# Optimization experiments

Hardware: AMD Instinct MI355X
Metric: run time of the kernel (lower is better)

## Reference

```python
import jax, jax.numpy as jnp
import numpy as np

N_NODES = 100000
N_EDGES = 1600000
D_IN = 128
D_OUT = 128


def setup_inputs() -> dict:
    key = jax.random.key(0)
    k1, k2, k3, k4 = jax.random.split(key, 4)
    x = jax.random.normal(k1, (N_NODES, D_IN), dtype=jnp.float32)
    # Xavier-uniform-like init for weight (exact distribution irrelevant for correctness baseline)
    weight = jax.random.normal(k2, (D_IN, D_OUT), dtype=jnp.float32) * (1.0 / np.sqrt(D_IN))
    bias = jnp.zeros((D_OUT,), dtype=jnp.float32)
    edge_index = jax.random.randint(k3, (2, N_EDGES), 0, N_NODES, dtype=jnp.int64 if jax.config.read('jax_enable_x64') else jnp.int32)
    edge_weight = jax.random.uniform(k4, (N_EDGES,), dtype=jnp.float32)
    return {"x": x, "weight": weight, "bias": bias,
            "edge_index": edge_index, "edge_weight": edge_weight}


def reference(x, weight, bias, edge_index, edge_weight):
    # support = X @ W   -- dense projection [N, D_out]
    support = x @ weight
    # output = A @ support -- SpMM via gather + weighted segment-sum
    src = edge_index[1]  # column index of adj (neighbor being aggregated)
    dst = edge_index[0]  # row index of adj (node receiving the message)
    messages = support[src] * edge_weight[:, None]          # [E, D_out]
    out = jax.ops.segment_sum(messages, dst, num_segments=N_NODES)  # [N, D_out]
    return out + bias
```

## Files before the change

kernel.cpp:

```cpp
#include <hip/hip_runtime.h>
#include <hip/hip_bf16.h>

#define N_NODES 100000
#define N_EDGES 1600000
#define D 128

#define NBUK 1024
#define BSH 7
#define CAP 2560
#define CAP_H 1344
#define NAGG2 (((N_NODES + 127) >> BSH) * 2)
#define NSCAT 512
#define PA_EPB 3125
#define SRC_MASK 0x01FFFFFF

typedef __attribute__((ext_vector_type(8))) short bf16x8;
typedef __attribute__((ext_vector_type(4))) float f32x4;

static __device__ __forceinline__ short f2bf(float f) {
    unsigned u = __builtin_bit_cast(unsigned, f);
    u += 0x7FFFu + ((u >> 16) & 1u);
    return (short)(u >> 16);
}
static __device__ __forceinline__ float bf2f(unsigned short h) {
    unsigned u = ((unsigned)h) << 16;
    return __builtin_bit_cast(float, u);
}

__global__ void wt_kernel(const float* __restrict__ w, short* __restrict__ wt,
                          int* __restrict__ gcur) {
    const int i = blockIdx.x * blockDim.x + threadIdx.x;
    if (i < D * D) {
        const int k = i / D, c = i % D;
        wt[c * D + k] = f2bf(w[i]);
    }
    if (i < NBUK) gcur[i] = 0;
}

__global__ __launch_bounds__(256) void gemm_mfma_kernel(
    const float* __restrict__ x, const short* __restrict__ wt,
    short* __restrict__ sup) {
    const int wid = blockIdx.x * 4 + (threadIdx.x >> 6);
    if (wid >= N_NODES / 16) return;
    const int l = threadIdx.x & 63;
    const int r = l & 15, g = l >> 4;
    const size_t row0 = (size_t)wid * 16;

    bf16x8 a[4];
    const float* xp = x + (row0 + r) * D + g * 8;
#pragma unroll
    for (int ks = 0; ks < 4; ++ks) {
        const float4 f0 = *reinterpret_cast<const float4*>(xp + ks * 32);
        const float4 f1 = *reinterpret_cast<const float4*>(xp + ks * 32 + 4);
        bf16x8 t;
        t[0] = f2bf(f0.x); t[1] = f2bf(f0.y); t[2] = f2bf(f0.z); t[3] = f2bf(f0.w);
        t[4] = f2bf(f1.x); t[5] = f2bf(f1.y); t[6] = f2bf(f1.z); t[7] = f2bf(f1.w);
        a[ks] = t;
    }

#pragma unroll
    for (int nt = 0; nt < 8; ++nt) {
        f32x4 acc = {0.f, 0.f, 0.f, 0.f};
        const short* wp = wt + (size_t)(nt * 16 + r) * D + g * 8;
#pragma unroll
        for (int ks = 0; ks < 4; ++ks) {
            const bf16x8 b = *reinterpret_cast<const bf16x8*>(wp + ks * 32);
            acc = __builtin_amdgcn_mfma_f32_16x16x32_bf16(a[ks], b, acc, 0, 0, 0);
        }
        short* sp = sup + (row0 + g * 4) * D + nt * 16 + r;
#pragma unroll
        for (int q = 0; q < 4; ++q) sp[q * D] = f2bf(acc[q]);
    }
}

__global__ __launch_bounds__(1024) void bukscatter_kernel(
    const int* __restrict__ dst, const int* __restrict__ src,
    const float* __restrict__ ew, int* __restrict__ gcur,
    int2* __restrict__ inter_sw) {
    __shared__ int h[NBUK];
    const int t = threadIdx.x;
    if (t < NBUK) h[t] = 0;
    __syncthreads();
    const int beg = blockIdx.x * PA_EPB;
    const int end = min(beg + PA_EPB, N_EDGES);
    for (int i = beg + t; i < end; i += 1024)
        atomicAdd(&h[dst[i] >> BSH], 1);
    __syncthreads();
    if (t < NBUK) {
        const int c = h[t];
        h[t] = c ? (t * CAP + atomicAdd(&gcur[t], c)) : 0;
    }
    __syncthreads();
    for (int i = beg + t; i < end; i += 1024) {
        const int d = dst[i];
        const int pos = atomicAdd(&h[d >> BSH], 1);
        inter_sw[pos] = make_int2(src[i] | ((d & 127) << 25),
                                  __float_as_int(ew[i]));
    }
}

__global__ __launch_bounds__(512) void sortagg_kernel(
    const int* __restrict__ gcur, const int2* __restrict__ inter_sw,
    const short* __restrict__ sup, const float* __restrict__ bias,
    float* __restrict__ out) {
    __shared__ int2 eb[CAP_H];
    __shared__ int st[64];
    __shared__ int cur[64];
    const int b = blockIdx.x, t = threadIdx.x;
    const int cb = b >> 1, hf = b & 1;
    const int cnt = gcur[cb];
    const int2* in = inter_sw + (size_t)cb * CAP;

    if (t < 64) st[t] = 0;
    __syncthreads();

    int2 e0, e1, e2, e3, e4;
    bool k0 = false, k1 = false, k2 = false, k3 = false, k4 = false;
    const int i0 = t, i1 = t + 512, i2 = t + 1024, i3 = t + 1536, i4 = t + 2048;
    if (i0 < cnt) { e0 = in[i0]; const int d7 = (unsigned)e0.x >> 25; if ((d7 >> 6) == hf) { k0 = true; atomicAdd(&st[d7 & 63], 1); } }
    if (i1 < cnt) { e1 = in[i1]; const int d7 = (unsigned)e1.x >> 25; if ((d7 >> 6) == hf) { k1 = true; atomicAdd(&st[d7 & 63], 1); } }
    if (i2 < cnt) { e2 = in[i2]; const int d7 = (unsigned)e2.x >> 25; if ((d7 >> 6) == hf) { k2 = true; atomicAdd(&st[d7 & 63], 1); } }
    if (i3 < cnt) { e3 = in[i3]; const int d7 = (unsigned)e3.x >> 25; if ((d7 >> 6) == hf) { k3 = true; atomicAdd(&st[d7 & 63], 1); } }
    if (i4 < cnt) { e4 = in[i4]; const int d7 = (unsigned)e4.x >> 25; if ((d7 >> 6) == hf) { k4 = true; atomicAdd(&st[d7 & 63], 1); } }
    __syncthreads();

    if (t < 64) {
        const int hv = st[t];
        int s = hv;
#pragma unroll
        for (int o = 1; o < 64; o <<= 1) {
            const int v = __shfl_up(s, o);
            if (t >= o) s += v;
        }
        st[t] = s - hv;
        cur[t] = s - hv;
    }
    __syncthreads();

    if (k0) eb[atomicAdd(&cur[((unsigned)e0.x >> 25) & 63], 1)] = make_int2(e0.x & SRC_MASK, e0.y);
    if (k1) eb[atomicAdd(&cur[((unsigned)e1.x >> 25) & 63], 1)] = make_int2(e1.x & SRC_MASK, e1.y);
    if (k2) eb[atomicAdd(&cur[((unsigned)e2.x >> 25) & 63], 1)] = make_int2(e2.x & SRC_MASK, e2.y);
    if (k3) eb[atomicAdd(&cur[((unsigned)e3.x >> 25) & 63], 1)] = make_int2(e3.x & SRC_MASK, e3.y);
    if (k4) eb[atomicAdd(&cur[((unsigned)e4.x >> 25) & 63], 1)] = make_int2(e4.x & SRC_MASK, e4.y);
    __syncthreads();

    const int wv = t >> 6, lane = t & 63;
    const int g = lane >> 4;
    const int fl = lane & 15;
    const int node0 = (cb << BSH) + (hf << 6);

    const float4 b0 = *reinterpret_cast<const float4*>(&bias[fl * 8]);
    const float4 b1 = *reinterpret_cast<const float4*>(&bias[fl * 8 + 4]);

    for (int k = 0; k < 8; ++k) {
        const int nl = wv * 8 + k;
        const int node = node0 + nl;
        if (node >= N_NODES) break;
        const int beg = st[nl], end = cur[nl];

        float acc[8] = {0, 0, 0, 0, 0, 0, 0, 0};
        for (int i = beg + g; i < end; i += 4) {
            const int2 sw = eb[i];
            const float w = __int_as_float(sw.y);
            const bf16x8 v = *reinterpret_cast<const bf16x8*>(
                &sup[(size_t)sw.x * D + fl * 8]);
#pragma unroll
            for (int q = 0; q < 8; ++q)
                acc[q] = fmaf(w, bf2f((unsigned short)v[q]), acc[q]);
        }
#pragma unroll
        for (int q = 0; q < 8; ++q) {
            acc[q] += __shfl_xor(acc[q], 16);
            acc[q] += __shfl_xor(acc[q], 32);
        }
        if (g == 0) {
            float* o = &out[(size_t)node * D + fl * 8];
            reinterpret_cast<float4*>(o)[0] =
                make_float4(acc[0] + b0.x, acc[1] + b0.y, acc[2] + b0.z, acc[3] + b0.w);
            reinterpret_cast<float4*>(o)[1] =
                make_float4(acc[4] + b1.x, acc[5] + b1.y, acc[6] + b1.z, acc[7] + b1.w);
        }
    }
}

extern "C" void kernel_launch(void* const* d_in, const int* in_sizes, int n_in,
                              void* d_out, int out_size, void* d_ws, size_t ws_size,
                              hipStream_t stream) {
    const float* x      = (const float*)d_in[0];
    const float* weight = (const float*)d_in[1];
    const float* bias   = (const float*)d_in[2];
    const int*   eidx   = (const int*)d_in[3];
    const float* ew     = (const float*)d_in[4];
    float* out = (float*)d_out;

    const int* dst_idx = eidx;
    const int* src_idx = eidx + N_EDGES;

    char* p = (char*)d_ws;
    short* sup       = (short*)p;  p += (size_t)N_NODES * D * 2;
    short* wt        = (short*)p;  p += (size_t)D * D * 2;
    int*   gcur      = (int*)p;    p += NBUK * 4;
    int2*  inter_sw  = (int2*)p;   p += (size_t)NBUK * CAP * 8;

    wt_kernel<<<(D * D + 255) / 256, 256, 0, stream>>>(weight, wt, gcur);

    gemm_mfma_kernel<<<(N_NODES / 16 + 3) / 4, 256, 0, stream>>>(x, wt, sup);

    bukscatter_kernel<<<NSCAT, 1024, 0, stream>>>(dst_idx, src_idx, ew, gcur,
                                                  inter_sw);

    sortagg_kernel<<<NAGG2, 512, 0, stream>>>(gcur, inter_sw, sup, bias, out);
}
```

Baseline: 134.2 us.

## Quantize projected features to int8 with per-row scales folded into edge weights

Adds a pass that quantizes the bf16 support matrix to int8 with a per-row absmax scale. The per-row scale is multiplied into each edge weight during bucket scatter, so the gather in aggregation reads 8 bytes per lane instead of 16. The aim is to halve gather traffic in the memory-bound SpMM. The cost is an extra kernel and a random scale lookup per edge in the scatter. The workspace is reorganized so inter_sw aliases the bf16 buffer, and the scatter block count is halved. Int8 quantization also loosens accuracy further than bf16.

```diff
diff --git a/kernel.cpp b/kernel.cpp
--- a/kernel.cpp
+++ b/kernel.cpp
@@ -10,8 +10,8 @@
 #define CAP 2560
 #define CAP_H 1344
 #define NAGG2 (((N_NODES + 127) >> BSH) * 2)
-#define NSCAT 512
-#define PA_EPB 3125
+#define NSCAT 256
+#define PA_EPB 6250
 #define SRC_MASK 0x01FFFFFF
 
 typedef __attribute__((ext_vector_type(8))) short bf16x8;
@@ -39,7 +39,7 @@
 
 __global__ __launch_bounds__(256) void gemm_mfma_kernel(
     const float* __restrict__ x, const short* __restrict__ wt,
-    short* __restrict__ sup) {
+    short* __restrict__ sup16) {
     const int wid = blockIdx.x * 4 + (threadIdx.x >> 6);
     if (wid >= N_NODES / 16) return;
     const int l = threadIdx.x & 63;
@@ -67,16 +67,40 @@
             const bf16x8 b = *reinterpret_cast<const bf16x8*>(wp + ks * 32);
             acc = __builtin_amdgcn_mfma_f32_16x16x32_bf16(a[ks], b, acc, 0, 0, 0);
         }
-        short* sp = sup + (row0 + g * 4) * D + nt * 16 + r;
+        short* sp = sup16 + (row0 + g * 4) * D + nt * 16 + r;
 #pragma unroll
         for (int q = 0; q < 4; ++q) sp[q * D] = f2bf(acc[q]);
     }
+}
+
+__global__ __launch_bounds__(256) void quant_kernel(
+    const short* __restrict__ sup16, signed char* __restrict__ sup8,
+    float* __restrict__ scales) {
+    const int row = blockIdx.x * 4 + (threadIdx.x >> 6);
+    if (row >= N_NODES) return;
+    const int lane = threadIdx.x & 63;
+
+    const unsigned v = *reinterpret_cast<const unsigned*>(
+        &sup16[(size_t)row * D + lane * 2]);
+    const float a = bf2f((unsigned short)(v & 0xFFFFu));
+    const float b = bf2f((unsigned short)(v >> 16));
+    float m = fmaxf(fabsf(a), fabsf(b));
+#pragma unroll
+    for (int o = 1; o < 64; o <<= 1) m = fmaxf(m, __shfl_xor(m, o));
+
+    const float inv = (m > 0.f) ? 127.f / m : 0.f;
+    const int qa = __float2int_rn(a * inv);
+    const int qb = __float2int_rn(b * inv);
+    const unsigned short packed =
+        (unsigned short)((qa & 0xFF) | ((qb & 0xFF) << 8));
+    *reinterpret_cast<unsigned short*>(&sup8[(size_t)row * D + lane * 2]) = packed;
+    if (lane == 0) scales[row] = m * (1.f / 127.f);
 }
 
 __global__ __launch_bounds__(1024) void bukscatter_kernel(
     const int* __restrict__ dst, const int* __restrict__ src,
-    const float* __restrict__ ew, int* __restrict__ gcur,
-    int2* __restrict__ inter_sw) {
+    const float* __restrict__ ew, const float* __restrict__ scales,
+    int* __restrict__ gcur, int2* __restrict__ inter_sw) {
     __shared__ int h[NBUK];
     const int t = threadIdx.x;
     if (t < NBUK) h[t] = 0;
@@ -93,15 +117,16 @@
     __syncthreads();
     for (int i = beg + t; i < end; i += 1024) {
         const int d = dst[i];
+        const int s = src[i];
         const int pos = atomicAdd(&h[d >> BSH], 1);
-        inter_sw[pos] = make_int2(src[i] | ((d & 127) << 25),
-                                  __float_as_int(ew[i]));
+        inter_sw[pos] = make_int2(s | ((d & 127) << 25),
+                                  __float_as_int(ew[i] * scales[s]));
     }
 }
 
 __global__ __launch_bounds__(512) void sortagg_kernel(
     const int* __restrict__ gcur, const int2* __restrict__ inter_sw,
-    const short* __restrict__ sup, const float* __restrict__ bias,
+    const signed char* __restrict__ sup8, const float* __restrict__ bias,
     float* __restrict__ out) {
     __shared__ int2 eb[CAP_H];
     __shared__ int st[64];
@@ -162,11 +187,12 @@
         for (int i = beg + g; i < end; i += 4) {
             const int2 sw = eb[i];
             const float w = __int_as_float(sw.y);
-            const bf16x8 v = *reinterpret_cast<const bf16x8*>(
-                &sup[(size_t)sw.x * D + fl * 8]);
+            const unsigned long long v =
+                *reinterpret_cast<const unsigned long long*>(
+                    &sup8[(size_t)sw.x * D + fl * 8]);
 #pragma unroll
             for (int q = 0; q < 8; ++q)
-                acc[q] = fmaf(w, bf2f((unsigned short)v[q]), acc[q]);
+                acc[q] = fmaf(w, (float)((signed char)(v >> (8 * q))), acc[q]);
         }
 #pragma unroll
         for (int q = 0; q < 8; ++q) {
@@ -197,17 +223,22 @@
     const int* src_idx = eidx + N_EDGES;
 
     char* p = (char*)d_ws;
-    short* sup       = (short*)p;  p += (size_t)N_NODES * D * 2;
+    short* sup16     = (short*)p;
+    int2*  inter_sw  = (int2*)p;
+    p += (size_t)N_NODES * D * 2;
+    signed char* sup8 = (signed char*)p; p += (size_t)N_NODES * D;
+    float* scales    = (float*)p;  p += (size_t)N_NODES * 4;
     short* wt        = (short*)p;  p += (size_t)D * D * 2;
     int*   gcur      = (int*)p;    p += NBUK * 4;
-    int2*  inter_sw  = (int2*)p;   p += (size_t)NBUK * CAP * 8;
 
     wt_kernel<<<(D * D + 255) / 256, 256, 0, stream>>>(weight, wt, gcur);
 
-    gemm_mfma_kernel<<<(N_NODES / 16 + 3) / 4, 256, 0, stream>>>(x, wt, sup);
-
-    bukscatter_kernel<<<NSCAT, 1024, 0, stream>>>(dst_idx, src_idx, ew, gcur,
-                                                  inter_sw);
-
-    sortagg_kernel<<<NAGG2, 512, 0, stream>>>(gcur, inter_sw, sup, bias, out);
-}
+    gemm_mfma_kernel<<<(N_NODES / 16 + 3) / 4, 256, 0, stream>>>(x, wt, sup16);
+
+    quant_kernel<<<(N_NODES + 3) / 4, 256, 0, stream>>>(sup16, sup8, scales);
+
+    bukscatter_kernel<<<NSCAT, 1024, 0, stream>>>(dst_idx, src_idx, ew, scales,
+                                                  gcur, inter_sw);
+
+    sortagg_kernel<<<NAGG2, 512, 0, stream>>>(gcur, inter_sw, sup8, bias, out);
+}
```

New measurement: 133.3 us. About the same (-0.7%).
